# Kernel optimization log

Hardware: AMD Instinct MI355X
Metric: run time of the kernel (lower is better)

The kernel has to match this reference:

```python
import jax, jax.numpy as jnp
import numpy as np

N_TOKENS = 8192
D_MODEL = 1024
HIDDEN = 4096   # d_model * expert_hidden_mult(4)
N_EXPERTS = 8
TOP_K = 2
LN_EPS = 1e-5


def setup_inputs() -> dict:
    key = jax.random.key(0)
    ks = jax.random.split(key, 8)
    s_in = 1.0 / np.sqrt(D_MODEL)
    s_h = 1.0 / np.sqrt(HIDDEN)
    return {
        "x": jax.random.normal(ks[0], (N_TOKENS, D_MODEL), jnp.float32),
        "Wr": jax.random.normal(ks[1], (D_MODEL, N_EXPERTS), jnp.float32) * s_in,
        "W1": jax.random.normal(ks[2], (N_EXPERTS, D_MODEL, HIDDEN), jnp.float32) * s_in,
        "b1": jnp.zeros((N_EXPERTS, HIDDEN), jnp.float32),
        "W2": jax.random.normal(ks[3], (N_EXPERTS, HIDDEN, D_MODEL), jnp.float32) * s_h,
        "b2": jnp.zeros((N_EXPERTS, D_MODEL), jnp.float32),
        "ln_w": jnp.ones((D_MODEL,), jnp.float32),
        "ln_b": jnp.zeros((D_MODEL,), jnp.float32),
    }


def reference(x, Wr, W1, b1, W2, b2, ln_w, ln_b):
    N, d = x.shape
    E = Wr.shape[1]
    # --- Router: top-k softmax gates scattered into dense [N, E] ---
    logits = x @ Wr                                   # [N, E]
    topv, topi = jax.lax.top_k(logits, TOP_K)         # [N, K]
    gv = jax.nn.softmax(topv, axis=-1)                # renormalized top-k gates
    gates = jnp.zeros_like(logits).at[jnp.arange(N)[:, None], topi].set(gv)
    # --- Experts: gate_e > 0 masks tokens; zero gate contributes zero, so
    # dense per-expert FFN weighted by the (mostly-zero) gate column is the
    # same math as the original gather/FFN/scatter-add dispatch. ---
    mixed = jnp.zeros_like(x)
    for e in range(E):  # small fixed expert count
        h = jax.nn.gelu(x @ W1[e] + b1[e])            # [N, HIDDEN]
        y = h @ W2[e] + b2[e]                         # [N, d]
        mixed = mixed + gates[:, e:e + 1] * y
    # --- Load-balancing aux loss (importance * load) ---
    importance = jnp.mean(jax.nn.softmax(logits, axis=-1), axis=0)  # [E]
    load = jnp.mean((gates > 0).astype(x.dtype), axis=0)            # [E]
    aux_loss = E * jnp.sum(importance * load)
    # --- Residual + LayerNorm (output_dropout is identity in eval) ---
    res = x + mixed
    mu = jnp.mean(res, axis=-1, keepdims=True)
    var = jnp.var(res, axis=-1, keepdims=True)
    out = (res - mu) * jax.lax.rsqrt(var + LN_EPS) * ln_w + ln_b
    return out, aux_loss
```

## Files before the change

kernel.cpp:

```cpp
#include <hip/hip_runtime.h>

#define N_TOK 8192
#define DM 1024
#define HID 4096
#define NE 8
#define MAX_TILES 136
#define MAX_SLOTS (MAX_TILES * 128)
#define LN_EPS 1e-5f

typedef __attribute__((ext_vector_type(8))) _Float16 f16x8;
typedef __attribute__((ext_vector_type(4))) _Float16 f16x4;
typedef __attribute__((ext_vector_type(4))) float f32x4;

constexpr size_t OFF_WT1 = 0;
constexpr size_t OFF_WT2 = OFF_WT1 + (size_t)NE * HID * DM * 2;
constexpr size_t OFF_XG  = OFF_WT2 + (size_t)NE * DM * HID * 2;
constexpr size_t OFF_H   = OFF_XG + (size_t)MAX_SLOTS * DM * 2;
constexpr size_t OFF_Y   = OFF_H + (size_t)MAX_SLOTS * HID * 2;
constexpr size_t OFF_TOPI = OFF_Y + (size_t)MAX_SLOTS * DM * 2;
constexpr size_t OFF_TOPG = OFF_TOPI + (size_t)N_TOK * 2 * 4;
constexpr size_t OFF_PTOK = OFF_TOPG + (size_t)N_TOK * 2 * 4;
constexpr size_t OFF_SLOT = OFF_PTOK + (size_t)MAX_SLOTS * 4;
constexpr size_t OFF_HDR = OFF_SLOT + (size_t)N_TOK * 2 * 4;
constexpr size_t WS_NEEDED = OFF_HDR + 4096;

__device__ inline float gelu_fast(float v) {
  float c = 0.7978845608028654f * (v + 0.044715f * v * v * v);
  return v / (1.0f + __expf(-2.0f * c));
}

__device__ inline void g2l16(const _Float16* g, _Float16* l) {
  __builtin_amdgcn_global_load_lds(
      (const __attribute__((address_space(1))) unsigned int*)g,
      (__attribute__((address_space(3))) unsigned int*)l, 16, 0, 0);
}

__global__ __launch_bounds__(256) void k_router(
    const float* __restrict__ x, const float* __restrict__ Wr,
    int* __restrict__ topi, float* __restrict__ topg,
    int* __restrict__ cnt, float* __restrict__ imp) {
  __shared__ float wr[DM * NE];
  __shared__ float blkImp[NE];
  __shared__ int blkCnt[NE];
  int tid = threadIdx.x;
  if (tid < NE) { blkImp[tid] = 0.0f; blkCnt[tid] = 0; }
  for (int i = tid; i < DM * NE / 4; i += 256)
    ((float4*)wr)[i] = ((const float4*)Wr)[i];
  __syncthreads();
  int wave = tid >> 6, lane = tid & 63;
  for (int it = 0; it < 4; ++it) {
    int t = blockIdx.x * 16 + wave * 4 + it;
    double acc[NE];
#pragma unroll
    for (int e = 0; e < NE; ++e) acc[e] = 0.0;
    for (int j = 0; j < DM / 64; ++j) {
      int d = j * 64 + lane;
      float xv = x[(size_t)t * DM + d];
#pragma unroll
      for (int e = 0; e < NE; ++e) acc[e] += (double)xv * (double)wr[d * NE + e];
    }
#pragma unroll
    for (int off = 32; off > 0; off >>= 1) {
#pragma unroll
      for (int e = 0; e < NE; ++e) acc[e] += __shfl_down(acc[e], off);
    }
    if (lane == 0) {
      int i0 = 0;
#pragma unroll
      for (int e = 1; e < NE; ++e) if (acc[e] > acc[i0]) i0 = e;
      int i1 = (i0 == 0) ? 1 : 0;
#pragma unroll
      for (int e = 0; e < NE; ++e) if (e != i0 && acc[e] > acc[i1]) i1 = e;
      double g0 = 1.0 / (1.0 + exp(acc[i1] - acc[i0]));
      topi[t * 2] = i0; topi[t * 2 + 1] = i1;
      topg[t * 2] = (float)g0; topg[t * 2 + 1] = (float)(1.0 - g0);
      atomicAdd(&blkCnt[i0], 1); atomicAdd(&blkCnt[i1], 1);
      double mx = acc[0];
#pragma unroll
      for (int e = 1; e < NE; ++e) mx = acc[e] > mx ? acc[e] : mx;
      double s = 0.0, p[NE];
#pragma unroll
      for (int e = 0; e < NE; ++e) { p[e] = exp(acc[e] - mx); s += p[e]; }
      double inv = 1.0 / s;
#pragma unroll
      for (int e = 0; e < NE; ++e) atomicAdd(&blkImp[e], (float)(p[e] * inv));
    }
  }
  __syncthreads();
  if (tid < NE) { atomicAdd(&cnt[tid], blkCnt[tid]); atomicAdd(&imp[tid], blkImp[tid]); }
}

__global__ void k_setup(int* __restrict__ hdr, float* __restrict__ aux_out) {
  int* cnt = hdr;
  float* imp = (float*)(hdr + 8);
  int* cursor = hdr + 16;
  int* off = hdr + 24;
  int* n_tiles_p = hdr + 33;
  int* tile_expert = hdr + 34;
  if (threadIdx.x == 0) {
    int offl[NE + 1];
    int o = 0;
    for (int e = 0; e < NE; ++e) {
      offl[e] = o; off[e] = o; cursor[e] = o;
      o += ((cnt[e] + 127) >> 7) << 7;
    }
    offl[NE] = o; off[NE] = o;
    int nt = o >> 7;
    *n_tiles_p = nt;
    int e = 0;
    for (int i = 0; i < nt; ++i) {
      while (i * 128 >= offl[e + 1]) ++e;
      tile_expert[i] = e;
    }
    double a = 0.0;
    for (int e2 = 0; e2 < NE; ++e2)
      a += ((double)imp[e2] / (double)N_TOK) * ((double)cnt[e2] / (double)N_TOK);
    *aux_out = (float)((double)NE * a);
  }
}

__global__ __launch_bounds__(256) void k_init_pairs(int* __restrict__ pair_token) {
  int i = blockIdx.x * 256 + threadIdx.x;
  if (i < MAX_SLOTS) pair_token[i] = -1;
}

__global__ __launch_bounds__(256) void k_scatter(
    const int* __restrict__ topi, int* __restrict__ cursor,
    int* __restrict__ pair_token, int* __restrict__ slot_of) {
  int t = blockIdx.x * 256 + threadIdx.x;
#pragma unroll
  for (int k = 0; k < 2; ++k) {
    int e = topi[t * 2 + k];
    int p = atomicAdd(&cursor[e], 1);
    pair_token[p] = t;
    slot_of[t * 2 + k] = p;
  }
}

__global__ __launch_bounds__(256) void k_gather(
    const float* __restrict__ x, const int* __restrict__ pair_token,
    _Float16* __restrict__ Xg) {
  int slot = blockIdx.x;
  int t = pair_token[slot];
  int d = threadIdx.x * 4;
  f16x4 v4 = {0, 0, 0, 0};
  if (t >= 0) {
    float4 v = *(const float4*)(x + (size_t)t * DM + d);
    v4[0] = (_Float16)v.x; v4[1] = (_Float16)v.y;
    v4[2] = (_Float16)v.z; v4[3] = (_Float16)v.w;
  }
  *(f16x4*)(Xg + (size_t)slot * DM + d) = v4;
}

__global__ __launch_bounds__(256) void k_transpose(
    const float* __restrict__ in, _Float16* __restrict__ out, int R, int C) {
  __shared__ float t[64 * 65];
  size_t base = (size_t)blockIdx.z * R * C;
  int c0 = blockIdx.x * 64, r0 = blockIdx.y * 64;
  int cx = (threadIdx.x & 15) * 4, ry = threadIdx.x >> 4;
#pragma unroll
  for (int p = 0; p < 4; ++p) {
    int r = p * 16 + ry;
    float4 v = *(const float4*)(in + base + (size_t)(r0 + r) * C + c0 + cx);
    t[r * 65 + cx] = v.x; t[r * 65 + cx + 1] = v.y;
    t[r * 65 + cx + 2] = v.z; t[r * 65 + cx + 3] = v.w;
  }
  __syncthreads();
#pragma unroll
  for (int q = 0; q < 2; ++q) {
    int lin = q * 256 + threadIdx.x;
    int c = lin >> 3, ch = lin & 7;
    f16x8 v;
#pragma unroll
    for (int j = 0; j < 8; ++j) v[j] = (_Float16)t[(ch * 8 + j) * 65 + c];
    *(f16x8*)(out + base + (size_t)(c0 + c) * R + r0 + ch * 8) = v;
  }
}

__device__ inline void stage_async(const _Float16* __restrict__ g, int ld,
                                   _Float16* __restrict__ l, int tid) {
  int wbase = tid & 192;
#pragma unroll
  for (int p = 0; p < 4; ++p) {
    int s = p * 256 + tid;
    int row = s >> 3;
    int c = (s & 7) ^ (row & 7);
    g2l16(g + (size_t)row * ld + c * 8, l + (size_t)(p * 256 + wbase) * 8);
  }
}

__device__ inline f16x8 lds_frag(const _Float16* __restrict__ l, int row, int cc) {
  return *(const f16x8*)(l + row * 64 + (((cc) ^ (row & 7)) << 3));
}

__global__ __launch_bounds__(256, 4) void k_gemm1(
    const _Float16* __restrict__ Xg, const _Float16* __restrict__ Wt1,
    const float* __restrict__ b1, _Float16* __restrict__ H,
    const int* __restrict__ hdr) {
  int tileM = blockIdx.y;
  if (tileM >= hdr[33]) return;
  int e = hdr[34 + tileM];
  int tileN = blockIdx.x;
  __shared__ _Float16 lds[2 * 128 * 64];
  _Float16* Al = lds;
  _Float16* Bl = lds + 128 * 64;
  int tid = threadIdx.x;
  const _Float16* Ag = Xg + (size_t)tileM * 128 * DM;
  const _Float16* Bg = Wt1 + (size_t)e * HID * DM + (size_t)tileN * 128 * DM;
  f32x4 acc[4][4];
  const f32x4 fz = {0.f, 0.f, 0.f, 0.f};
#pragma unroll
  for (int a = 0; a < 4; ++a)
#pragma unroll
    for (int b = 0; b < 4; ++b) acc[a][b] = fz;
  int wave = tid >> 6, lane = tid & 63;
  int wm = wave & 1, wn = wave >> 1;
  int l16 = lane & 15, quad = lane >> 4;
  for (int k0 = 0; k0 < DM; k0 += 64) {
    stage_async(Ag + k0, DM, Al, tid);
    stage_async(Bg + k0, DM, Bl, tid);
    __syncthreads();
#pragma unroll
    for (int kk = 0; kk < 64; kk += 32) {
      f16x8 af[4], bfr[4];
      int cc = quad + (kk >> 3);
#pragma unroll
      for (int mi = 0; mi < 4; ++mi)
        af[mi] = lds_frag(Al, wm * 64 + mi * 16 + l16, cc);
#pragma unroll
      for (int ni = 0; ni < 4; ++ni)
        bfr[ni] = lds_frag(Bl, wn * 64 + ni * 16 + l16, cc);
#pragma unroll
      for (int mi = 0; mi < 4; ++mi)
#pragma unroll
        for (int ni = 0; ni < 4; ++ni)
          acc[mi][ni] = __builtin_amdgcn_mfma_f32_16x16x32_f16(af[mi], bfr[ni], acc[mi][ni], 0, 0, 0);
    }
    __syncthreads();
  }
  int rowBase = tileM * 128 + wm * 64;
  int colBase = tileN * 128 + wn * 64;
  _Float16* sc = lds + wave * 4096;
  float bv[4];
#pragma unroll
  for (int ni = 0; ni < 4; ++ni) bv[ni] = b1[e * HID + colBase + ni * 16 + l16];
#pragma unroll
  for (int mi = 0; mi < 4; ++mi)
#pragma unroll
    for (int ni = 0; ni < 4; ++ni)
#pragma unroll
      for (int i = 0; i < 4; ++i) {
        int r = mi * 16 + quad * 4 + i;
        int c = ni * 16 + l16;
        sc[r * 64 + c] = (_Float16)gelu_fast(acc[mi][ni][i] + bv[ni]);
      }
  __syncthreads();
#pragma unroll
  for (int j = 0; j < 8; ++j) {
    int lin = j * 64 + lane;
    int r = lin >> 3, ch = lin & 7;
    f16x8 v = *(const f16x8*)(sc + r * 64 + ch * 8);
    *(f16x8*)(H + (size_t)(rowBase + r) * HID + colBase + ch * 8) = v;
  }
}

__global__ __launch_bounds__(256, 4) void k_gemm2(
    const _Float16* __restrict__ H, const _Float16* __restrict__ Wt2,
    const float* __restrict__ b2, _Float16* __restrict__ Y,
    const int* __restrict__ hdr) {
  int tileM = blockIdx.y;
  if (tileM >= hdr[33]) return;
  int e = hdr[34 + tileM];
  int tileN = blockIdx.x;
  __shared__ _Float16 lds[2 * 128 * 64];
  _Float16* Al = lds;
  _Float16* Bl = lds + 128 * 64;
  int tid = threadIdx.x;
  const _Float16* Ag = H + (size_t)tileM * 128 * HID;
  const _Float16* Bg = Wt2 + (size_t)e * DM * HID + (size_t)tileN * 128 * HID;
  f32x4 acc[4][4];
  const f32x4 fz = {0.f, 0.f, 0.f, 0.f};
#pragma unroll
  for (int a = 0; a < 4; ++a)
#pragma unroll
    for (int b = 0; b < 4; ++b) acc[a][b] = fz;
  int wave = tid >> 6, lane = tid & 63;
  int wm = wave & 1, wn = wave >> 1;
  int l16 = lane & 15, quad = lane >> 4;
  for (int k0 = 0; k0 < HID; k0 += 64) {
    stage_async(Ag + k0, HID, Al, tid);
    stage_async(Bg + k0, HID, Bl, tid);
    __syncthreads();
#pragma unroll
    for (int kk = 0; kk < 64; kk += 32) {
      f16x8 af[4], bfr[4];
      int cc = quad + (kk >> 3);
#pragma unroll
      for (int mi = 0; mi < 4; ++mi)
        af[mi] = lds_frag(Al, wm * 64 + mi * 16 + l16, cc);
#pragma unroll
      for (int ni = 0; ni < 4; ++ni)
        bfr[ni] = lds_frag(Bl, wn * 64 + ni * 16 + l16, cc);
#pragma unroll
      for (int mi = 0; mi < 4; ++mi)
#pragma unroll
        for (int ni = 0; ni < 4; ++ni)
          acc[mi][ni] = __builtin_amdgcn_mfma_f32_16x16x32_f16(af[mi], bfr[ni], acc[mi][ni], 0, 0, 0);
    }
    __syncthreads();
  }
  int rowBase = tileM * 128 + wm * 64;
  int colBase = tileN * 128 + wn * 64;
  _Float16* sc = lds + wave * 4096;
  float bv[4];
#pragma unroll
  for (int ni = 0; ni < 4; ++ni) bv[ni] = b2[e * DM + colBase + ni * 16 + l16];
#pragma unroll
  for (int mi = 0; mi < 4; ++mi)
#pragma unroll
    for (int ni = 0; ni < 4; ++ni)
#pragma unroll
      for (int i = 0; i < 4; ++i) {
        int r = mi * 16 + quad * 4 + i;
        int c = ni * 16 + l16;
        sc[r * 64 + c] = (_Float16)(acc[mi][ni][i] + bv[ni]);
      }
  __syncthreads();
#pragma unroll
  for (int j = 0; j < 8; ++j) {
    int lin = j * 64 + lane;
    int r = lin >> 3, ch = lin & 7;
    f16x8 v = *(const f16x8*)(sc + r * 64 + ch * 8);
    *(f16x8*)(Y + (size_t)(rowBase + r) * DM + colBase + ch * 8) = v;
  }
}

__global__ __launch_bounds__(256) void k_ln(
    const float* __restrict__ x, const _Float16* __restrict__ Y,
    const int* __restrict__ slot_of, const float* __restrict__ topg,
    const float* __restrict__ lnw, const float* __restrict__ lnb,
    float* __restrict__ out) {
  int t = blockIdx.x, tid = threadIdx.x;
  int s0 = slot_of[t * 2], s1 = slot_of[t * 2 + 1];
  float g0 = topg[t * 2], g1 = topg[t * 2 + 1];
  float4 xv = ((const float4*)(x + (size_t)t * DM))[tid];
  f16x4 y0 = ((const f16x4*)(Y + (size_t)s0 * DM))[tid];
  f16x4 y1 = ((const f16x4*)(Y + (size_t)s1 * DM))[tid];
  float r0 = xv.x + g0 * (float)y0[0] + g1 * (float)y1[0];
  float r1 = xv.y + g0 * (float)y0[1] + g1 * (float)y1[1];
  float r2 = xv.z + g0 * (float)y0[2] + g1 * (float)y1[2];
  float r3 = xv.w + g0 * (float)y0[3] + g1 * (float)y1[3];
  float s = r0 + r1 + r2 + r3;
  float s2 = r0 * r0 + r1 * r1 + r2 * r2 + r3 * r3;
#pragma unroll
  for (int off = 32; off > 0; off >>= 1) {
    s += __shfl_down(s, off);
    s2 += __shfl_down(s2, off);
  }
  __shared__ float ss[4], ss2[4];
  int wave = tid >> 6, lane = tid & 63;
  if (lane == 0) { ss[wave] = s; ss2[wave] = s2; }
  __syncthreads();
  float S = ss[0] + ss[1] + ss[2] + ss[3];
  float S2 = ss2[0] + ss2[1] + ss2[2] + ss2[3];
  float mu = S * (1.0f / DM);
  float var = S2 * (1.0f / DM) - mu * mu;
  float inv = rsqrtf(var + LN_EPS);
  float4 wv = ((const float4*)lnw)[tid];
  float4 bv = ((const float4*)lnb)[tid];
  float4 o;
  o.x = (r0 - mu) * inv * wv.x + bv.x;
  o.y = (r1 - mu) * inv * wv.y + bv.y;
  o.z = (r2 - mu) * inv * wv.z + bv.z;
  o.w = (r3 - mu) * inv * wv.w + bv.w;
  ((float4*)(out + (size_t)t * DM))[tid] = o;
}

__global__ void k_sentinel(float* out, float v) { out[threadIdx.x] = v; }

extern "C" void kernel_launch(void* const* d_in, const int* in_sizes, int n_in,
                              void* d_out, int out_size, void* d_ws, size_t ws_size,
                              hipStream_t stream) {
  const float* x = (const float*)d_in[0];
  const float* Wr = (const float*)d_in[1];
  const float* W1 = (const float*)d_in[2];
  const float* b1 = (const float*)d_in[3];
  const float* W2 = (const float*)d_in[4];
  const float* b2 = (const float*)d_in[5];
  const float* lnw = (const float*)d_in[6];
  const float* lnb = (const float*)d_in[7];
  float* out = (float*)d_out;
  char* ws = (char*)d_ws;

  if (ws_size < WS_NEEDED) {
    k_sentinel<<<1, 256, 0, stream>>>(out, 1.0e6f + (float)(ws_size >> 20));
    return;
  }

  _Float16* Wt1 = (_Float16*)(ws + OFF_WT1);
  _Float16* Wt2 = (_Float16*)(ws + OFF_WT2);
  _Float16* Xg = (_Float16*)(ws + OFF_XG);
  _Float16* Hbuf = (_Float16*)(ws + OFF_H);
  _Float16* Ybuf = (_Float16*)(ws + OFF_Y);
  int* topi = (int*)(ws + OFF_TOPI);
  float* topg = (float*)(ws + OFF_TOPG);
  int* pair_token = (int*)(ws + OFF_PTOK);
  int* slot_of = (int*)(ws + OFF_SLOT);
  int* hdr = (int*)(ws + OFF_HDR);
  int* cnt = hdr;
  float* imp = (float*)(hdr + 8);
  int* cursor = hdr + 16;

  hipMemsetAsync(hdr, 0, 64, stream);

  k_transpose<<<dim3(HID / 64, DM / 64, NE), 256, 0, stream>>>(W1, Wt1, DM, HID);
  k_transpose<<<dim3(DM / 64, HID / 64, NE), 256, 0, stream>>>(W2, Wt2, HID, DM);
  k_router<<<512, 256, 0, stream>>>(x, Wr, topi, topg, cnt, imp);
  k_setup<<<1, 1, 0, stream>>>(hdr, out + (size_t)N_TOK * DM);
  k_init_pairs<<<(MAX_SLOTS + 255) / 256, 256, 0, stream>>>(pair_token);
  k_scatter<<<N_TOK / 256, 256, 0, stream>>>(topi, cursor, pair_token, slot_of);
  k_gather<<<MAX_SLOTS, 256, 0, stream>>>(x, pair_token, Xg);
  k_gemm1<<<dim3(HID / 128, MAX_TILES), 256, 0, stream>>>(Xg, Wt1, b1, Hbuf, hdr);
  k_gemm2<<<dim3(DM / 128, MAX_TILES), 256, 0, stream>>>(Hbuf, Wt2, b2, Ybuf, hdr);
  k_ln<<<N_TOK, 256, 0, stream>>>(x, Ybuf, slot_of, topg, lnw, lnb, out);
}
```

Baseline: 852.8 us.

## Merge expert GEMMs into templated 128x256 tile kernel with XCD-aware block remap

```diff
diff --git a/kernel.cpp b/kernel.cpp
--- a/kernel.cpp
+++ b/kernel.cpp
@@ -193,145 +193,86 @@
   return *(const f16x8*)(l + row * 64 + (((cc) ^ (row & 7)) << 3));
 }
 
-__global__ __launch_bounds__(256, 4) void k_gemm1(
-    const _Float16* __restrict__ Xg, const _Float16* __restrict__ Wt1,
-    const float* __restrict__ b1, _Float16* __restrict__ H,
+template <int KD, int ND, bool GELU>
+__global__ __launch_bounds__(256, 2) void k_ffn(
+    const _Float16* __restrict__ A, const _Float16* __restrict__ Bw,
+    const float* __restrict__ bias, _Float16* __restrict__ C,
     const int* __restrict__ hdr) {
-  int tileM = blockIdx.y;
+  constexpr int GX = ND / 256;
+  constexpr int NWG = GX * MAX_TILES;
+  constexpr int Q = NWG >> 3;
+  constexpr int R = NWG & 7;
+  int orig = blockIdx.y * GX + blockIdx.x;
+  int xcd = orig & 7, loc = orig >> 3;
+  int wg = (xcd < R ? xcd * (Q + 1) : R * (Q + 1) + (xcd - R) * Q) + loc;
+  int tileM = wg / GX, tileN = wg % GX;
   if (tileM >= hdr[33]) return;
   int e = hdr[34 + tileM];
-  int tileN = blockIdx.x;
-  __shared__ _Float16 lds[2 * 128 * 64];
+  __shared__ _Float16 lds[(128 + 256) * 64];
   _Float16* Al = lds;
   _Float16* Bl = lds + 128 * 64;
   int tid = threadIdx.x;
-  const _Float16* Ag = Xg + (size_t)tileM * 128 * DM;
-  const _Float16* Bg = Wt1 + (size_t)e * HID * DM + (size_t)tileN * 128 * DM;
-  f32x4 acc[4][4];
+  const _Float16* Ag = A + (size_t)tileM * 128 * KD;
+  const _Float16* Bg = Bw + (size_t)e * ND * KD + (size_t)tileN * 256 * KD;
+  f32x4 acc[8][4];
   const f32x4 fz = {0.f, 0.f, 0.f, 0.f};
 #pragma unroll
-  for (int a = 0; a < 4; ++a)
+  for (int a = 0; a < 8; ++a)
 #pragma unroll
     for (int b = 0; b < 4; ++b) acc[a][b] = fz;
   int wave = tid >> 6, lane = tid & 63;
-  int wm = wave & 1, wn = wave >> 1;
   int l16 = lane & 15, quad = lane >> 4;
-  for (int k0 = 0; k0 < DM; k0 += 64) {
-    stage_async(Ag + k0, DM, Al, tid);
-    stage_async(Bg + k0, DM, Bl, tid);
+  for (int k0 = 0; k0 < KD; k0 += 64) {
+    stage_async(Ag + k0, KD, Al, tid);
+    stage_async(Bg + k0, KD, Bl, tid);
+    stage_async(Bg + (size_t)128 * KD + k0, KD, Bl + 128 * 64, tid);
     __syncthreads();
 #pragma unroll
     for (int kk = 0; kk < 64; kk += 32) {
-      f16x8 af[4], bfr[4];
       int cc = quad + (kk >> 3);
-#pragma unroll
-      for (int mi = 0; mi < 4; ++mi)
-        af[mi] = lds_frag(Al, wm * 64 + mi * 16 + l16, cc);
+      f16x8 af[8], bf[4];
+#pragma unroll
+      for (int mi = 0; mi < 8; ++mi)
+        af[mi] = lds_frag(Al, mi * 16 + l16, cc);
 #pragma unroll
       for (int ni = 0; ni < 4; ++ni)
-        bfr[ni] = lds_frag(Bl, wn * 64 + ni * 16 + l16, cc);
-#pragma unroll
-      for (int mi = 0; mi < 4; ++mi)
+        bf[ni] = lds_frag(Bl, wave * 64 + ni * 16 + l16, cc);
+#pragma unroll
+      for (int mi = 0; mi < 8; ++mi)
 #pragma unroll
         for (int ni = 0; ni < 4; ++ni)
-          acc[mi][ni] = __builtin_amdgcn_mfma_f32_16x16x32_f16(af[mi], bfr[ni], acc[mi][ni], 0, 0, 0);
+          acc[mi][ni] = __builtin_amdgcn_mfma_f32_16x16x32_f16(af[mi], bf[ni], acc[mi][ni], 0, 0, 0);
     }
     __syncthreads();
   }
-  int rowBase = tileM * 128 + wm * 64;
-  int colBase = tileN * 128 + wn * 64;
+  int rowBase = tileM * 128;
+  int colBase = tileN * 256 + wave * 64;
   _Float16* sc = lds + wave * 4096;
   float bv[4];
 #pragma unroll
-  for (int ni = 0; ni < 4; ++ni) bv[ni] = b1[e * HID + colBase + ni * 16 + l16];
-#pragma unroll
-  for (int mi = 0; mi < 4; ++mi)
-#pragma unroll
-    for (int ni = 0; ni < 4; ++ni)
-#pragma unroll
-      for (int i = 0; i < 4; ++i) {
-        int r = mi * 16 + quad * 4 + i;
-        int c = ni * 16 + l16;
-        sc[r * 64 + c] = (_Float16)gelu_fast(acc[mi][ni][i] + bv[ni]);
-      }
-  __syncthreads();
-#pragma unroll
-  for (int j = 0; j < 8; ++j) {
-    int lin = j * 64 + lane;
-    int r = lin >> 3, ch = lin & 7;
-    f16x8 v = *(const f16x8*)(sc + r * 64 + ch * 8);
-    *(f16x8*)(H + (size_t)(rowBase + r) * HID + colBase + ch * 8) = v;
-  }
-}
-
-__global__ __launch_bounds__(256, 4) void k_gemm2(
-    const _Float16* __restrict__ H, const _Float16* __restrict__ Wt2,
-    const float* __restrict__ b2, _Float16* __restrict__ Y,
-    const int* __restrict__ hdr) {
-  int tileM = blockIdx.y;
-  if (tileM >= hdr[33]) return;
-  int e = hdr[34 + tileM];
-  int tileN = blockIdx.x;
-  __shared__ _Float16 lds[2 * 128 * 64];
-  _Float16* Al = lds;
-  _Float16* Bl = lds + 128 * 64;
-  int tid = threadIdx.x;
-  const _Float16* Ag = H + (size_t)tileM * 128 * HID;
-  const _Float16* Bg = Wt2 + (size_t)e * DM * HID + (size_t)tileN * 128 * HID;
-  f32x4 acc[4][4];
-  const f32x4 fz = {0.f, 0.f, 0.f, 0.f};
-#pragma unroll
-  for (int a = 0; a < 4; ++a)
-#pragma unroll
-    for (int b = 0; b < 4; ++b) acc[a][b] = fz;
-  int wave = tid >> 6, lane = tid & 63;
-  int wm = wave & 1, wn = wave >> 1;
-  int l16 = lane & 15, quad = lane >> 4;
-  for (int k0 = 0; k0 < HID; k0 += 64) {
-    stage_async(Ag + k0, HID, Al, tid);
-    stage_async(Bg + k0, HID, Bl, tid);
+  for (int ni = 0; ni < 4; ++ni) bv[ni] = bias[e * ND + colBase + ni * 16 + l16];
+#pragma unroll
+  for (int h = 0; h < 2; ++h) {
+#pragma unroll
+    for (int mi = 0; mi < 4; ++mi)
+#pragma unroll
+      for (int ni = 0; ni < 4; ++ni)
+#pragma unroll
+        for (int i = 0; i < 4; ++i) {
+          int rr = mi * 16 + quad * 4 + i;
+          int c2 = ni * 16 + l16;
+          float v = acc[h * 4 + mi][ni][i] + bv[ni];
+          sc[rr * 64 + c2] = (_Float16)(GELU ? gelu_fast(v) : v);
+        }
     __syncthreads();
 #pragma unroll
-    for (int kk = 0; kk < 64; kk += 32) {
-      f16x8 af[4], bfr[4];
-      int cc = quad + (kk >> 3);
-#pragma unroll
-      for (int mi = 0; mi < 4; ++mi)
-        af[mi] = lds_frag(Al, wm * 64 + mi * 16 + l16, cc);
-#pragma unroll
-      for (int ni = 0; ni < 4; ++ni)
-        bfr[ni] = lds_frag(Bl, wn * 64 + ni * 16 + l16, cc);
-#pragma unroll
-      for (int mi = 0; mi < 4; ++mi)
-#pragma unroll
-        for (int ni = 0; ni < 4; ++ni)
-          acc[mi][ni] = __builtin_amdgcn_mfma_f32_16x16x32_f16(af[mi], bfr[ni], acc[mi][ni], 0, 0, 0);
+    for (int j = 0; j < 8; ++j) {
+      int lin = j * 64 + lane;
+      int rr = lin >> 3, ch = lin & 7;
+      f16x8 v = *(const f16x8*)(sc + rr * 64 + ch * 8);
+      *(f16x8*)(C + (size_t)(rowBase + h * 64 + rr) * ND + colBase + ch * 8) = v;
     }
     __syncthreads();
-  }
-  int rowBase = tileM * 128 + wm * 64;
-  int colBase = tileN * 128 + wn * 64;
-  _Float16* sc = lds + wave * 4096;
-  float bv[4];
-#pragma unroll
-  for (int ni = 0; ni < 4; ++ni) bv[ni] = b2[e * DM + colBase + ni * 16 + l16];
-#pragma unroll
-  for (int mi = 0; mi < 4; ++mi)
-#pragma unroll
-    for (int ni = 0; ni < 4; ++ni)
-#pragma unroll
-      for (int i = 0; i < 4; ++i) {
-        int r = mi * 16 + quad * 4 + i;
-        int c = ni * 16 + l16;
-        sc[r * 64 + c] = (_Float16)(acc[mi][ni][i] + bv[ni]);
-      }
-  __syncthreads();
-#pragma unroll
-  for (int j = 0; j < 8; ++j) {
-    int lin = j * 64 + lane;
-    int r = lin >> 3, ch = lin & 7;
-    f16x8 v = *(const f16x8*)(sc + r * 64 + ch * 8);
-    *(f16x8*)(Y + (size_t)(rowBase + r) * DM + colBase + ch * 8) = v;
   }
 }
 
@@ -420,7 +361,7 @@
   k_init_pairs<<<(MAX_SLOTS + 255) / 256, 256, 0, stream>>>(pair_token);
   k_scatter<<<N_TOK / 256, 256, 0, stream>>>(topi, cursor, pair_token, slot_of);
   k_gather<<<MAX_SLOTS, 256, 0, stream>>>(x, pair_token, Xg);
-  k_gemm1<<<dim3(HID / 128, MAX_TILES), 256, 0, stream>>>(Xg, Wt1, b1, Hbuf, hdr);
-  k_gemm2<<<dim3(DM / 128, MAX_TILES), 256, 0, stream>>>(Hbuf, Wt2, b2, Ybuf, hdr);
+  k_ffn<DM, HID, true><<<dim3(HID / 256, MAX_TILES), 256, 0, stream>>>(Xg, Wt1, b1, Hbuf, hdr);
+  k_ffn<HID, DM, false><<<dim3(DM / 256, MAX_TILES), 256, 0, stream>>>(Hbuf, Wt2, b2, Ybuf, hdr);
   k_ln<<<N_TOK, 256, 0, stream>>>(x, Ybuf, slot_of, topg, lnw, lnb, out);
 }
```

Result: slower. 885.7 us (+3.9%).
